# Optimization experiments

Measured on AMD Instinct MI355X. Metric: run time of the kernel, lower is better.

The kernel has to match this reference:

```python
import jax, jax.numpy as jnp
import numpy as np

T, Z, D_DIM = 8, 2048, 1024
N_EXP, P_SLOT, H = 64, 32, 1024
LN_EPS = 1e-5


def setup_inputs() -> dict:
    key = jax.random.key(0)
    k = jax.random.split(key, 5)
    s = 0.02
    return {
        "x": jax.random.normal(k[0], (T, Z, D_DIM), dtype=jnp.float32),
        "phi_w": jax.random.normal(k[1], (N_EXP * P_SLOT, D_DIM), dtype=jnp.float32) * s,
        "phi_b": jax.random.normal(k[2], (N_EXP * P_SLOT,), dtype=jnp.float32) * s,
        "expert_w": jax.random.normal(k[3], (N_EXP, D_DIM, H), dtype=jnp.float32) * s,
        "expert_b": jax.random.normal(k[4], (N_EXP, H), dtype=jnp.float32) * s,
    }


def reference(x, phi_w, phi_b, expert_w, expert_b):
    t, z, d = x.shape
    n = expert_w.shape[0]
    p = phi_w.shape[0] // n
    # routing logits: [t, z, n, p]
    logits = (jnp.einsum('tzd,ed->tze', x, phi_w) + phi_b).reshape(t, z, n, p)
    D = jax.nn.softmax(logits, axis=3)  # dispatch: softmax over slots p
    C = jax.nn.softmax(logits, axis=2)  # combine:  softmax over experts n
    # slot inputs, summed over batch AND tokens (as in the source einsum)
    X_tilde = jnp.einsum('tznp,tzd->npd', D, x)
    X_tilde = jnp.clip(X_tilde, -33000.0, 65000.0)
    # layer norm over last dim, no affine
    mu = jnp.mean(X_tilde, axis=-1, keepdims=True)
    var = jnp.mean(jnp.square(X_tilde - mu), axis=-1, keepdims=True)
    X_tilde = (X_tilde - mu) * jax.lax.rsqrt(var + LN_EPS)
    X_tilde = jnp.tanh(X_tilde)
    # per-expert Linear, batched over experts: [n,p,d] x [n,d,H] -> [n,p,H]
    Y_tilde = jnp.einsum('npd,ndH->npH', X_tilde, expert_w) + expert_b[:, None, :]
    # combine back to tokens: [t,z,H]
    Y = jnp.einsum('tznp,npH->tzH', C, Y_tilde)
    return Y
```

## Files before the change

### kernel.cpp

```cpp
#include <hip/hip_runtime.h>
#include <hip/hip_bf16.h>
#include <math.h>

#define TOKENS   16384
#define DDIM     1024
#define NEXP     64
#define PSLOT    32
#define NSLOTS   2048
#define HDIM     1024
#define LN_EPS   1e-5f
#define KSPLIT   8

typedef __bf16 b16x8 __attribute__((ext_vector_type(8)));
typedef float  f32x4 __attribute__((ext_vector_type(4)));

__device__ __forceinline__ unsigned short f2b(float f) {
    union { float f; unsigned u; } v; v.f = f;
    unsigned r = v.u + 0x7FFF + ((v.u >> 16) & 1);
    return (unsigned short)(r >> 16);
}

__device__ __forceinline__ void load_lds16(const void* g, void* l) {
    __builtin_amdgcn_global_load_lds(
        (const __attribute__((address_space(1))) void*)g,
        (__attribute__((address_space(3))) void*)l, 16, 0, 0);
}

template<bool BIAS>
__global__ __launch_bounds__(512, 2) void gemm_nt_256(
    const unsigned short* __restrict__ A,
    const unsigned short* __restrict__ B,
    const float* __restrict__ bias,
    float* __restrict__ C,
    int M, int N, int K)
{
    __shared__ unsigned short lds[2][2][256 * 64];
    const int tid  = threadIdx.x;
    const int wave = tid >> 6;
    const int lane = tid & 63;
    const int wr = wave >> 2;
    const int wc = wave & 3;
    const int fr = lane & 15;
    const int fs = lane >> 4;
    const int kswz = ((lane & 7) ^ (lane >> 3)) * 8;

    const int gx  = (int)gridDim.x, gy = (int)gridDim.y;
    const int nwg = gx * gy;
    const int wg  = (int)blockIdx.y * gx + (int)blockIdx.x;
    const int swz = (wg & 7) * (nwg >> 3) + (wg >> 3);
    const int m0 = (swz / gx) * 256;
    const int n0 = (swz % gx) * 256;

    const int kc = K / gridDim.z;
    const int kb = blockIdx.z * kc;
    C += (size_t)blockIdx.z * M * N;
    const int NT = kc >> 6;

    f32x4 acc[8][4] = {};
    b16x8 Ag[4][2], Bf[2][2], Bs2[2][2];

#define KOF(T)   (kb + (T) * 64)

#define STAGE_A(BUF, T, R0) { \
    const int k0_ = KOF(T); \
    _Pragma("unroll") for (int hh = 0; hh < 2; ++hh) { \
        const int rp_ = (R0) + hh * 64 + wave * 8 + (lane >> 3); \
        const int L_  = ((rp_ >> 6) & 1) * 128 + ((rp_ >> 7) & 1) * 64 + (rp_ & 63); \
        load_lds16(A + (size_t)(m0 + L_) * K + k0_ + kswz, \
                   &lds[BUF][0][((R0) + hh * 64 + wave * 8) * 64]); } }

#define STAGE_B(BUF, T, R0) { \
    const int k0_ = KOF(T); \
    _Pragma("unroll") for (int hh = 0; hh < 2; ++hh) { \
        const int rp_ = (R0) + hh * 64 + wave * 8 + (lane >> 3); \
        const int L_  = ((rp_ >> 5) & 3) * 64 + ((rp_ >> 7) & 1) * 32 + (rp_ & 31); \
        load_lds16(B + (size_t)(n0 + L_) * K + k0_ + kswz, \
                   &lds[BUF][1][((R0) + hh * 64 + wave * 8) * 64]); } }

#define LDA_G(BUF, IBASE) \
    _Pragma("unroll") for (int ii = 0; ii < 4; ++ii) { \
        const int rp_ = (IBASE) + 64 * wr + ii * 16 + fr; \
        _Pragma("unroll") for (int h = 0; h < 2; ++h) \
            Ag[ii][h] = *(const b16x8*)&lds[BUF][0][rp_ * 64 + (((h * 4 + fs) ^ (rp_ & 7)) * 8)]; }

#define LDB_G(BUF, JBASE, DST) \
    _Pragma("unroll") for (int jj = 0; jj < 2; ++jj) { \
        const int rp_ = (JBASE) + 32 * wc + jj * 16 + fr; \
        _Pragma("unroll") for (int h = 0; h < 2; ++h) \
            DST[jj][h] = *(const b16x8*)&lds[BUF][1][rp_ * 64 + (((h * 4 + fs) ^ (rp_ & 7)) * 8)]; }

#define MFMA_Q(IB, JB, BREG) \
    __builtin_amdgcn_s_setprio(1); \
    _Pragma("unroll") for (int ii = 0; ii < 4; ++ii) \
    _Pragma("unroll") for (int jj = 0; jj < 2; ++jj) \
    _Pragma("unroll") for (int h = 0; h < 2; ++h) \
        acc[(IB) + ii][(JB) + jj] = __builtin_amdgcn_mfma_f32_16x16x32_bf16( \
            Ag[ii][h], BREG[jj][h], acc[(IB) + ii][(JB) + jj], 0, 0, 0); \
    __builtin_amdgcn_s_setprio(0);

#define BAR1  { __builtin_amdgcn_s_barrier(); __builtin_amdgcn_sched_barrier(0); }
#define BAR2  { __builtin_amdgcn_s_barrier(); }
#define VMW6  { asm volatile("s_waitcnt vmcnt(6)" ::: "memory"); \
                __builtin_amdgcn_sched_barrier(0); }
#define VMW0  { asm volatile("s_waitcnt vmcnt(0)" ::: "memory"); \
                __builtin_amdgcn_sched_barrier(0); }

    STAGE_A(0, 0, 0);   STAGE_B(0, 0, 0);   STAGE_B(0, 0, 128);  STAGE_A(0, 0, 128);
    STAGE_A(1, 1, 0);   STAGE_B(1, 1, 0);   STAGE_B(1, 1, 128);
    VMW6; BAR2;

    const int nit = NT >> 1;
    for (int it = 0; it < nit - 1; ++it) {
        const int t1 = 2 * it + 1;
        LDA_G(0, 0); LDB_G(0, 0, Bf);
        STAGE_A(1, t1, 128);
        BAR1; MFMA_Q(0, 0, Bf); BAR2;
        LDB_G(0, 128, Bs2);
        STAGE_A(0, t1 + 1, 0);
        BAR1; MFMA_Q(0, 2, Bs2); BAR2;
        LDA_G(0, 128);
        STAGE_B(0, t1 + 1, 0);
        BAR1; MFMA_Q(4, 2, Bs2); BAR2;
        STAGE_B(0, t1 + 1, 128);
        BAR1; MFMA_Q(4, 0, Bf); VMW6; BAR2;
        LDA_G(1, 0); LDB_G(1, 0, Bf);
        STAGE_A(0, t1 + 1, 128);
        BAR1; MFMA_Q(0, 0, Bf); BAR2;
        LDB_G(1, 128, Bs2);
        STAGE_A(1, t1 + 2, 0);
        BAR1; MFMA_Q(0, 2, Bs2); BAR2;
        LDA_G(1, 128);
        STAGE_B(1, t1 + 2, 0);
        BAR1; MFMA_Q(4, 2, Bs2); BAR2;
        STAGE_B(1, t1 + 2, 128);
        BAR1; MFMA_Q(4, 0, Bf); VMW6; BAR2;
    }

    {
        const int t1 = NT - 1;
        LDA_G(0, 0); LDB_G(0, 0, Bf);
        STAGE_A(1, t1, 128);
        BAR1; MFMA_Q(0, 0, Bf); BAR2;
        LDB_G(0, 128, Bs2);
        BAR1; MFMA_Q(0, 2, Bs2); BAR2;
        LDA_G(0, 128);
        BAR1; MFMA_Q(4, 2, Bs2); BAR2;
        BAR1; MFMA_Q(4, 0, Bf); VMW0; BAR2;
        LDA_G(1, 0); LDB_G(1, 0, Bf);
        BAR1; MFMA_Q(0, 0, Bf); BAR2;
        LDB_G(1, 128, Bs2);
        BAR1; MFMA_Q(0, 2, Bs2); BAR2;
        LDA_G(1, 128);
        BAR1; MFMA_Q(4, 2, Bs2); BAR2;
        BAR1; MFMA_Q(4, 0, Bf); BAR2;
    }

    const int col  = lane & 15;
    const int row4 = (lane >> 4) * 4;
#pragma unroll
    for (int j = 0; j < 4; ++j) {
        const int n = n0 + wc * 64 + j * 16 + col;
        const float bj = BIAS ? bias[n] : 0.f;
#pragma unroll
        for (int i = 0; i < 8; ++i) {
#pragma unroll
            for (int r = 0; r < 4; ++r) {
                const int m = m0 + wr * 128 + i * 16 + row4 + r;
                C[(size_t)m * N + n] = acc[i][j][r] + bj;
            }
        }
    }
#undef KOF
#undef STAGE_A
#undef STAGE_B
#undef LDA_G
#undef LDB_G
#undef MFMA_Q
#undef BAR1
#undef BAR2
#undef VMW6
#undef VMW0
}

__global__ __launch_bounds__(256) void prep_x(
    const float* __restrict__ in, unsigned short* __restrict__ xb,
    unsigned short* __restrict__ xT)
{
    __shared__ unsigned short tile[64][68];
    const int t  = threadIdx.x;
    const int c0 = blockIdx.x * 64;
    const int r0 = blockIdx.y * 64;
    const int tr = t >> 4, tc4 = (t & 15) * 4;
#pragma unroll
    for (int i = 0; i < 4; ++i) {
        const int r = tr + i * 16;
        const float4 v = *(const float4*)&in[(size_t)(r0 + r) * DDIM + c0 + tc4];
        ushort4 o;
        o.x = f2b(v.x); o.y = f2b(v.y); o.z = f2b(v.z); o.w = f2b(v.w);
        *(ushort4*)&xb[(size_t)(r0 + r) * DDIM + c0 + tc4] = o;
        tile[tc4 + 0][r] = o.x; tile[tc4 + 1][r] = o.y;
        tile[tc4 + 2][r] = o.z; tile[tc4 + 3][r] = o.w;
    }
    __syncthreads();
#pragma unroll
    for (int i = 0; i < 4; ++i) {
        const int r = tr + i * 16;
        ushort4 o;
        o.x = tile[r][tc4 + 0]; o.y = tile[r][tc4 + 1];
        o.z = tile[r][tc4 + 2]; o.w = tile[r][tc4 + 3];
        *(ushort4*)&xT[(size_t)(c0 + r) * TOKENS + r0 + tc4] = o;
    }
}

__global__ __launch_bounds__(256) void cast_f32_bf16(
    const float* __restrict__ in, unsigned short* __restrict__ out)
{
    const size_t i = (size_t)(blockIdx.x * 256 + threadIdx.x) * 8;
    const float4 a = *(const float4*)&in[i];
    const float4 b = *(const float4*)&in[i + 4];
    ushort4 o0, o1;
    o0.x = f2b(a.x); o0.y = f2b(a.y); o0.z = f2b(a.z); o0.w = f2b(a.w);
    o1.x = f2b(b.x); o1.y = f2b(b.y); o1.z = f2b(b.z); o1.w = f2b(b.w);
    *(ushort4*)&out[i]     = o0;
    *(ushort4*)&out[i + 4] = o1;
}

__global__ __launch_bounds__(256) void softmax_both(
    const float* __restrict__ logits,
    unsigned short* __restrict__ DbT, unsigned short* __restrict__ Cb)
{
    __shared__ float ls[8][32][33];
    __shared__ float Mv[32][33], Sv[32][33];
    const int tid  = threadIdx.x;
    const int tok0 = blockIdx.x * 32;
    const int tok  = tid & 31;

    {
        const int tk = tid >> 3, pp = (tid & 7) * 4;
#pragma unroll
        for (int q = 0; q < 4; ++q) { Mv[tk][pp + q] = -1e30f; Sv[tk][pp + q] = 0.f; }
    }
    __syncthreads();

    for (int c = 0; c < 8; ++c) {
#pragma unroll
        for (int i = 0; i < 8; ++i) {
            const int flat = i * 256 + tid;
            const int row  = flat >> 6;
            const int c4   = (flat & 63) * 4;
            const float4 v = *(const float4*)&logits[(size_t)(tok0 + row) * NSLOTS + c * 256 + c4];
            float* b = &ls[c4 >> 5][row][c4 & 31];
            b[0] = v.x; b[1] = v.y; b[2] = v.z; b[3] = v.w;
        }
        __syncthreads();

        {
            const int nl = tid >> 5;
            const float* r = ls[nl][tok];
            float m = r[0];
#pragma unroll
            for (int p = 1; p < PSLOT; ++p) m = fmaxf(m, r[p]);
            float s = 0.f;
#pragma unroll
            for (int p = 0; p < PSLOT; ++p) s += __expf(r[p] - m);
            const float inv = 1.f / s;
            unsigned short* o = &DbT[(size_t)(c * 256 + nl * 32) * TOKENS + tok0 + tok];
#pragma unroll
            for (int p = 0; p < PSLOT; ++p)
                o[(size_t)p * TOKENS] = f2b(__expf(r[p] - m) * inv);
        }

        {
            const int pg = tid >> 5;
#pragma unroll
            for (int k = 0; k < 4; ++k) {
                const int p = pg * 4 + k;
                float m8 = ls[0][tok][p];
#pragma unroll
                for (int n = 1; n < 8; ++n) m8 = fmaxf(m8, ls[n][tok][p]);
                float s8 = 0.f;
#pragma unroll
                for (int n = 0; n < 8; ++n) s8 += __expf(ls[n][tok][p] - m8);
                const float M = Mv[tok][p], S = Sv[tok][p];
                const float Mn = fmaxf(M, m8);
                Sv[tok][p] = S * __expf(M - Mn) + s8 * __expf(m8 - Mn);
                Mv[tok][p] = Mn;
            }
        }
        __syncthreads();
    }

    {
        const int tk = tid >> 3, pp = (tid & 7) * 4;
#pragma unroll
        for (int q = 0; q < 4; ++q) Sv[tk][pp + q] = 1.f / Sv[tk][pp + q];
    }
    __syncthreads();

    for (int c = 0; c < 8; ++c) {
#pragma unroll
        for (int i = 0; i < 8; ++i) {
            const int flat = i * 256 + tid;
            const int row  = flat >> 6;
            const int c4   = (flat & 63) * 4;
            const int p    = c4 & 31;
            const float4 v = *(const float4*)&logits[(size_t)(tok0 + row) * NSLOTS + c * 256 + c4];
            ushort4 o;
            o.x = f2b(__expf(v.x - Mv[row][p + 0]) * Sv[row][p + 0]);
            o.y = f2b(__expf(v.y - Mv[row][p + 1]) * Sv[row][p + 1]);
            o.z = f2b(__expf(v.z - Mv[row][p + 2]) * Sv[row][p + 2]);
            o.w = f2b(__expf(v.w - Mv[row][p + 3]) * Sv[row][p + 3]);
            *(ushort4*)&Cb[(size_t)(tok0 + row) * NSLOTS + c * 256 + c4] = o;
        }
    }
}

__global__ __launch_bounds__(256) void reduce_ln_tanh(
    const float* __restrict__ parts, float* __restrict__ Xt)
{
    const int tid = threadIdx.x;
    const size_t off = (size_t)blockIdx.x * DDIM + tid * 4;
    __shared__ float red1[4], red2[4];

    float4 v = *(const float4*)&parts[off];
#pragma unroll
    for (int s = 1; s < KSPLIT; ++s) {
        const float4 p = *(const float4*)&parts[(size_t)s * NSLOTS * DDIM + off];
        v.x += p.x; v.y += p.y; v.z += p.z; v.w += p.w;
    }
    v.x = fminf(fmaxf(v.x, -33000.f), 65000.f);
    v.y = fminf(fmaxf(v.y, -33000.f), 65000.f);
    v.z = fminf(fmaxf(v.z, -33000.f), 65000.f);
    v.w = fminf(fmaxf(v.w, -33000.f), 65000.f);

    float s = v.x + v.y + v.z + v.w;
#pragma unroll
    for (int off2 = 32; off2 > 0; off2 >>= 1) s += __shfl_down(s, off2);
    if ((tid & 63) == 0) red1[tid >> 6] = s;
    __syncthreads();
    const float mu = (red1[0] + red1[1] + red1[2] + red1[3]) * (1.f / DDIM);

    const float dx = v.x - mu, dy = v.y - mu, dz = v.z - mu, dw = v.w - mu;
    float q = dx * dx + dy * dy + dz * dz + dw * dw;
#pragma unroll
    for (int off2 = 32; off2 > 0; off2 >>= 1) q += __shfl_down(q, off2);
    if ((tid & 63) == 0) red2[tid >> 6] = q;
    __syncthreads();
    const float var = (red2[0] + red2[1] + red2[2] + red2[3]) * (1.f / DDIM);
    const float sc = rsqrtf(var + LN_EPS);

    float4 o;
    o.x = tanhf(dx * sc); o.y = tanhf(dy * sc);
    o.z = tanhf(dz * sc); o.w = tanhf(dw * sc);
    *(float4*)&Xt[off] = o;
}

__global__ __launch_bounds__(256) void expert_gemm(
    const float* __restrict__ Xt, const float* __restrict__ W,
    const float* __restrict__ bias, unsigned short* __restrict__ YtT)
{
    const int n   = blockIdx.y;
    const int h0  = blockIdx.x * 64;
    const int tid = threadIdx.x;
    __shared__ float As[32][17];
    __shared__ float Bs[16][68];
    __shared__ unsigned short ty[64][36];

    const int r  = tid >> 3;
    const int c8 = (tid & 7) * 8;
    float acc[8];
#pragma unroll
    for (int j = 0; j < 8; ++j) acc[j] = 0.f;

    const float* Wn = W + (size_t)n * DDIM * HDIM;
    for (int k0 = 0; k0 < DDIM; k0 += 16) {
        if (tid < 128) {
            const int row = tid >> 2, c4 = (tid & 3) * 4;
            const float4 v = *(const float4*)&Xt[(size_t)(n * 32 + row) * DDIM + k0 + c4];
            As[row][c4 + 0] = v.x; As[row][c4 + 1] = v.y;
            As[row][c4 + 2] = v.z; As[row][c4 + 3] = v.w;
        }
        {
            const int row = tid >> 4, c4 = (tid & 15) * 4;
            *(float4*)&Bs[row][c4] =
                *(const float4*)&Wn[(size_t)(k0 + row) * HDIM + h0 + c4];
        }
        __syncthreads();
#pragma unroll
        for (int kk = 0; kk < 16; ++kk) {
            const float a = As[r][kk];
            const float4 b0 = *(const float4*)&Bs[kk][c8];
            const float4 b1 = *(const float4*)&Bs[kk][c8 + 4];
            acc[0] = fmaf(a, b0.x, acc[0]); acc[1] = fmaf(a, b0.y, acc[1]);
            acc[2] = fmaf(a, b0.z, acc[2]); acc[3] = fmaf(a, b0.w, acc[3]);
            acc[4] = fmaf(a, b1.x, acc[4]); acc[5] = fmaf(a, b1.y, acc[5]);
            acc[6] = fmaf(a, b1.z, acc[6]); acc[7] = fmaf(a, b1.w, acc[7]);
        }
        __syncthreads();
    }

    const float* bn = bias + (size_t)n * HDIM + h0;
#pragma unroll
    for (int j = 0; j < 8; ++j)
        ty[c8 + j][r] = f2b(acc[j] + bn[c8 + j]);
    __syncthreads();

    const int row = tid >> 2, q = (tid & 3) * 8;
    const ushort4 u0 = *(const ushort4*)&ty[row][q];
    const ushort4 u1 = *(const ushort4*)&ty[row][q + 4];
    unsigned short* dst = &YtT[(size_t)(h0 + row) * NSLOTS + n * 32 + q];
    *(ushort4*)&dst[0] = u0;
    *(ushort4*)&dst[4] = u1;
}

extern "C" void kernel_launch(void* const* d_in, const int* in_sizes, int n_in,
                              void* d_out, int out_size, void* d_ws, size_t ws_size,
                              hipStream_t stream)
{
    const float* x        = (const float*)d_in[0];
    const float* phi_w    = (const float*)d_in[1];
    const float* phi_b    = (const float*)d_in[2];
    const float* expert_w = (const float*)d_in[3];
    const float* expert_b = (const float*)d_in[4];
    float* out = (float*)d_out;

    char* ws = (char*)d_ws;
    const size_t MB = 1u << 20;
    unsigned short* xb     = (unsigned short*)(ws);
    unsigned short* xT     = (unsigned short*)(ws +  32 * MB);
    unsigned short* pwb    = (unsigned short*)(ws +  64 * MB);
    float*          logits = (float*)(ws +  68 * MB);
    unsigned short* DbT    = (unsigned short*)(ws + 196 * MB);
    unsigned short* Cb     = (unsigned short*)(ws + 260 * MB);
    float*          parts  = (float*)(ws + 324 * MB);
    float*          Xt     = (float*)(ws + 388 * MB);
    unsigned short* YtT    = (unsigned short*)(ws + 396 * MB);

    prep_x<<<dim3(DDIM / 64, TOKENS / 64), 256, 0, stream>>>(x, xb, xT);
    cast_f32_bf16<<<NSLOTS * DDIM / (256 * 8), 256, 0, stream>>>(phi_w, pwb);

    gemm_nt_256<true><<<dim3(NSLOTS / 256, TOKENS / 256), 512, 0, stream>>>(
        xb, pwb, phi_b, logits, TOKENS, NSLOTS, DDIM);

    softmax_both<<<TOKENS / 32, 256, 0, stream>>>(logits, DbT, Cb);

    gemm_nt_256<false>
        <<<dim3(DDIM / 256, NSLOTS / 256, KSPLIT), 512, 0, stream>>>(
            DbT, xT, nullptr, parts, NSLOTS, DDIM, TOKENS);

    reduce_ln_tanh<<<NSLOTS, 256, 0, stream>>>(parts, Xt);

    expert_gemm<<<dim3(HDIM / 64, NEXP), 256, 0, stream>>>(
        Xt, expert_w, expert_b, YtT);

    gemm_nt_256<false><<<dim3(HDIM / 256, TOKENS / 256), 512, 0, stream>>>(
        Cb, YtT, nullptr, out, TOKENS, HDIM, NSLOTS);
}
```

Measured before the change: 767.4 us.

## Store routing logits as bf16 and double-buffer expert GEMM with direct LDS loads

The logits GEMM now writes bf16 instead of fp32, and the softmax kernel reads bf16 and widens it. This halves the 128MB logits write and its two reads. Separately, the expert GEMM tile grows to 32x128 with a K-step of 32, and it uses double-buffered global_load_lds staging with explicit vmcnt waits to overlap loads with FMA work. The cost is reduced logit precision before both softmaxes, plus more LDS and register use in the expert kernel.

```diff
diff --git a/kernel.cpp b/kernel.cpp
--- a/kernel.cpp
+++ b/kernel.cpp
@@ -19,6 +19,9 @@
     unsigned r = v.u + 0x7FFF + ((v.u >> 16) & 1);
     return (unsigned short)(r >> 16);
 }
+__device__ __forceinline__ float b2f(unsigned short u) {
+    union { unsigned u; float f; } v; v.u = ((unsigned)u) << 16; return v.f;
+}
 
 __device__ __forceinline__ void load_lds16(const void* g, void* l) {
     __builtin_amdgcn_global_load_lds(
@@ -26,12 +29,12 @@
         (__attribute__((address_space(3))) void*)l, 16, 0, 0);
 }
 
-template<bool BIAS>
+template<bool BIAS, typename OT>
 __global__ __launch_bounds__(512, 2) void gemm_nt_256(
     const unsigned short* __restrict__ A,
     const unsigned short* __restrict__ B,
     const float* __restrict__ bias,
-    float* __restrict__ C,
+    OT* __restrict__ C,
     int M, int N, int K)
 {
     __shared__ unsigned short lds[2][2][256 * 64];
@@ -166,7 +169,9 @@
 #pragma unroll
             for (int r = 0; r < 4; ++r) {
                 const int m = m0 + wr * 128 + i * 16 + row4 + r;
-                C[(size_t)m * N + n] = acc[i][j][r] + bj;
+                const float v = acc[i][j][r] + bj;
+                if constexpr (sizeof(OT) == 2) C[(size_t)m * N + n] = f2b(v);
+                else                            C[(size_t)m * N + n] = v;
             }
         }
     }
@@ -226,7 +231,7 @@
 }
 
 __global__ __launch_bounds__(256) void softmax_both(
-    const float* __restrict__ logits,
+    const unsigned short* __restrict__ logits,
     unsigned short* __restrict__ DbT, unsigned short* __restrict__ Cb)
 {
     __shared__ float ls[8][32][33];
@@ -244,13 +249,16 @@
 
     for (int c = 0; c < 8; ++c) {
 #pragma unroll
-        for (int i = 0; i < 8; ++i) {
+        for (int i = 0; i < 4; ++i) {
             const int flat = i * 256 + tid;
-            const int row  = flat >> 6;
-            const int c4   = (flat & 63) * 4;
-            const float4 v = *(const float4*)&logits[(size_t)(tok0 + row) * NSLOTS + c * 256 + c4];
-            float* b = &ls[c4 >> 5][row][c4 & 31];
-            b[0] = v.x; b[1] = v.y; b[2] = v.z; b[3] = v.w;
+            const int row  = flat >> 5;
+            const int c8   = (flat & 31) * 8;
+            const unsigned short* p = &logits[(size_t)(tok0 + row) * NSLOTS + c * 256 + c8];
+            const ushort4 u0 = *(const ushort4*)&p[0];
+            const ushort4 u1 = *(const ushort4*)&p[4];
+            float* b = &ls[c8 >> 5][row][c8 & 31];
+            b[0] = b2f(u0.x); b[1] = b2f(u0.y); b[2] = b2f(u0.z); b[3] = b2f(u0.w);
+            b[4] = b2f(u1.x); b[5] = b2f(u1.y); b[6] = b2f(u1.z); b[7] = b2f(u1.w);
         }
         __syncthreads();
 
@@ -299,18 +307,26 @@
 
     for (int c = 0; c < 8; ++c) {
 #pragma unroll
-        for (int i = 0; i < 8; ++i) {
+        for (int i = 0; i < 4; ++i) {
             const int flat = i * 256 + tid;
-            const int row  = flat >> 6;
-            const int c4   = (flat & 63) * 4;
-            const int p    = c4 & 31;
-            const float4 v = *(const float4*)&logits[(size_t)(tok0 + row) * NSLOTS + c * 256 + c4];
-            ushort4 o;
-            o.x = f2b(__expf(v.x - Mv[row][p + 0]) * Sv[row][p + 0]);
-            o.y = f2b(__expf(v.y - Mv[row][p + 1]) * Sv[row][p + 1]);
-            o.z = f2b(__expf(v.z - Mv[row][p + 2]) * Sv[row][p + 2]);
-            o.w = f2b(__expf(v.w - Mv[row][p + 3]) * Sv[row][p + 3]);
-            *(ushort4*)&Cb[(size_t)(tok0 + row) * NSLOTS + c * 256 + c4] = o;
+            const int row  = flat >> 5;
+            const int c8   = (flat & 31) * 8;
+            const int p    = c8 & 31;
+            const unsigned short* q = &logits[(size_t)(tok0 + row) * NSLOTS + c * 256 + c8];
+            const ushort4 u0 = *(const ushort4*)&q[0];
+            const ushort4 u1 = *(const ushort4*)&q[4];
+            ushort4 o0, o1;
+            o0.x = f2b(__expf(b2f(u0.x) - Mv[row][p + 0]) * Sv[row][p + 0]);
+            o0.y = f2b(__expf(b2f(u0.y) - Mv[row][p + 1]) * Sv[row][p + 1]);
+            o0.z = f2b(__expf(b2f(u0.z) - Mv[row][p + 2]) * Sv[row][p + 2]);
+            o0.w = f2b(__expf(b2f(u0.w) - Mv[row][p + 3]) * Sv[row][p + 3]);
+            o1.x = f2b(__expf(b2f(u1.x) - Mv[row][p + 4]) * Sv[row][p + 4]);
+            o1.y = f2b(__expf(b2f(u1.y) - Mv[row][p + 5]) * Sv[row][p + 5]);
+            o1.z = f2b(__expf(b2f(u1.z) - Mv[row][p + 6]) * Sv[row][p + 6]);
+            o1.w = f2b(__expf(b2f(u1.w) - Mv[row][p + 7]) * Sv[row][p + 7]);
+            unsigned short* d = &Cb[(size_t)(tok0 + row) * NSLOTS + c * 256 + c8];
+            *(ushort4*)&d[0] = o0;
+            *(ushort4*)&d[4] = o1;
         }
     }
 }
@@ -360,57 +376,75 @@
     const float* __restrict__ bias, unsigned short* __restrict__ YtT)
 {
     const int n   = blockIdx.y;
-    const int h0  = blockIdx.x * 64;
+    const int h0  = blockIdx.x * 128;
     const int tid = threadIdx.x;
-    __shared__ float As[32][17];
-    __shared__ float Bs[16][68];
-    __shared__ unsigned short ty[64][36];
-
-    const int r  = tid >> 3;
-    const int c8 = (tid & 7) * 8;
-    float acc[8];
-#pragma unroll
-    for (int j = 0; j < 8; ++j) acc[j] = 0.f;
+    __shared__ float As[2][32][32];
+    __shared__ float Bs[2][32][128];
+    __shared__ unsigned short ty[128][36];
+
+    const int r  = tid >> 4;
+    const int c8 = (tid & 15) * 8;
+    float acc0[8], acc1[8];
+#pragma unroll
+    for (int j = 0; j < 8; ++j) { acc0[j] = 0.f; acc1[j] = 0.f; }
 
     const float* Wn = W + (size_t)n * DDIM * HDIM;
-    for (int k0 = 0; k0 < DDIM; k0 += 16) {
-        if (tid < 128) {
-            const int row = tid >> 2, c4 = (tid & 3) * 4;
-            const float4 v = *(const float4*)&Xt[(size_t)(n * 32 + row) * DDIM + k0 + c4];
-            As[row][c4 + 0] = v.x; As[row][c4 + 1] = v.y;
-            As[row][c4 + 2] = v.z; As[row][c4 + 3] = v.w;
-        }
-        {
-            const int row = tid >> 4, c4 = (tid & 15) * 4;
-            *(float4*)&Bs[row][c4] =
-                *(const float4*)&Wn[(size_t)(k0 + row) * HDIM + h0 + c4];
-        }
-        __syncthreads();
-#pragma unroll
-        for (int kk = 0; kk < 16; ++kk) {
-            const float a = As[r][kk];
-            const float4 b0 = *(const float4*)&Bs[kk][c8];
-            const float4 b1 = *(const float4*)&Bs[kk][c8 + 4];
-            acc[0] = fmaf(a, b0.x, acc[0]); acc[1] = fmaf(a, b0.y, acc[1]);
-            acc[2] = fmaf(a, b0.z, acc[2]); acc[3] = fmaf(a, b0.w, acc[3]);
-            acc[4] = fmaf(a, b1.x, acc[4]); acc[5] = fmaf(a, b1.y, acc[5]);
-            acc[6] = fmaf(a, b1.z, acc[6]); acc[7] = fmaf(a, b1.w, acc[7]);
-        }
-        __syncthreads();
-    }
+    const float* Xn = Xt + (size_t)n * 32 * DDIM;
+
+#define EG_STAGE(T, BUF) { \
+    const int k0_ = (T) * 32; \
+    _Pragma("unroll") for (int i = 0; i < 4; ++i) { \
+        const int flat = i * 256 + tid; \
+        const int brow = flat >> 5, bch = (flat & 31) * 4; \
+        load_lds16(Wn + (size_t)(k0_ + brow) * HDIM + h0 + bch, \
+                   &Bs[BUF][brow][bch]); } \
+    { const int arow = tid >> 3, ach = (tid & 7) * 4; \
+      load_lds16(Xn + (size_t)arow * DDIM + k0_ + ach, &As[BUF][arow][ach]); } }
+
+    EG_STAGE(0, 0);
+    for (int t = 0; t < 32; ++t) {
+        const int buf = t & 1;
+        if (t < 31) {
+            EG_STAGE(t + 1, (t + 1) & 1);
+            asm volatile("s_waitcnt vmcnt(5)" ::: "memory");
+        } else {
+            asm volatile("s_waitcnt vmcnt(0)" ::: "memory");
+        }
+        __builtin_amdgcn_sched_barrier(0);
+        __builtin_amdgcn_s_barrier();
+#pragma unroll
+        for (int kk = 0; kk < 32; ++kk) {
+            const float a0 = As[buf][r][kk];
+            const float a1 = As[buf][r + 16][kk];
+            const float4 b0 = *(const float4*)&Bs[buf][kk][c8];
+            const float4 b1 = *(const float4*)&Bs[buf][kk][c8 + 4];
+            acc0[0] = fmaf(a0, b0.x, acc0[0]); acc0[1] = fmaf(a0, b0.y, acc0[1]);
+            acc0[2] = fmaf(a0, b0.z, acc0[2]); acc0[3] = fmaf(a0, b0.w, acc0[3]);
+            acc0[4] = fmaf(a0, b1.x, acc0[4]); acc0[5] = fmaf(a0, b1.y, acc0[5]);
+            acc0[6] = fmaf(a0, b1.z, acc0[6]); acc0[7] = fmaf(a0, b1.w, acc0[7]);
+            acc1[0] = fmaf(a1, b0.x, acc1[0]); acc1[1] = fmaf(a1, b0.y, acc1[1]);
+            acc1[2] = fmaf(a1, b0.z, acc1[2]); acc1[3] = fmaf(a1, b0.w, acc1[3]);
+            acc1[4] = fmaf(a1, b1.x, acc1[4]); acc1[5] = fmaf(a1, b1.y, acc1[5]);
+            acc1[6] = fmaf(a1, b1.z, acc1[6]); acc1[7] = fmaf(a1, b1.w, acc1[7]);
+        }
+        __builtin_amdgcn_s_barrier();
+    }
+#undef EG_STAGE
 
     const float* bn = bias + (size_t)n * HDIM + h0;
 #pragma unroll
-    for (int j = 0; j < 8; ++j)
-        ty[c8 + j][r] = f2b(acc[j] + bn[c8 + j]);
-    __syncthreads();
-
-    const int row = tid >> 2, q = (tid & 3) * 8;
-    const ushort4 u0 = *(const ushort4*)&ty[row][q];
-    const ushort4 u1 = *(const ushort4*)&ty[row][q + 4];
+    for (int j = 0; j < 8; ++j) {
+        const float bj = bn[c8 + j];
+        ty[c8 + j][r]      = f2b(acc0[j] + bj);
+        ty[c8 + j][r + 16] = f2b(acc1[j] + bj);
+    }
+    __syncthreads();
+
+    const int row = tid >> 1, q = (tid & 1) * 16;
     unsigned short* dst = &YtT[(size_t)(h0 + row) * NSLOTS + n * 32 + q];
-    *(ushort4*)&dst[0] = u0;
-    *(ushort4*)&dst[4] = u1;
+#pragma unroll
+    for (int u = 0; u < 4; ++u)
+        *(ushort4*)&dst[u * 4] = *(const ushort4*)&ty[row][q + u * 4];
 }
 
 extern "C" void kernel_launch(void* const* d_in, const int* in_sizes, int n_in,
@@ -429,30 +463,32 @@
     unsigned short* xb     = (unsigned short*)(ws);
     unsigned short* xT     = (unsigned short*)(ws +  32 * MB);
     unsigned short* pwb    = (unsigned short*)(ws +  64 * MB);
-    float*          logits = (float*)(ws +  68 * MB);
-    unsigned short* DbT    = (unsigned short*)(ws + 196 * MB);
-    unsigned short* Cb     = (unsigned short*)(ws + 260 * MB);
-    float*          parts  = (float*)(ws + 324 * MB);
-    float*          Xt     = (float*)(ws + 388 * MB);
-    unsigned short* YtT    = (unsigned short*)(ws + 396 * MB);
+    unsigned short* logbf  = (unsigned short*)(ws +  68 * MB);
+    unsigned short* DbT    = (unsigned short*)(ws + 132 * MB);
+    unsigned short* Cb     = (unsigned short*)(ws + 196 * MB);
+    float*          parts  = (float*)(ws + 260 * MB);
+    float*          Xt     = (float*)(ws + 324 * MB);
+    unsigned short* YtT    = (unsigned short*)(ws + 332 * MB);
 
     prep_x<<<dim3(DDIM / 64, TOKENS / 64), 256, 0, stream>>>(x, xb, xT);
     cast_f32_bf16<<<NSLOTS * DDIM / (256 * 8), 256, 0, stream>>>(phi_w, pwb);
 
-    gemm_nt_256<true><<<dim3(NSLOTS / 256, TOKENS / 256), 512, 0, stream>>>(
-        xb, pwb, phi_b, logits, TOKENS, NSLOTS, DDIM);
-
-    softmax_both<<<TOKENS / 32, 256, 0, stream>>>(logits, DbT, Cb);
-
-    gemm_nt_256<false>
+    gemm_nt_256<true, unsigned short>
+        <<<dim3(NSLOTS / 256, TOKENS / 256), 512, 0, stream>>>(
+            xb, pwb, phi_b, logbf, TOKENS, NSLOTS, DDIM);
+
+    softmax_both<<<TOKENS / 32, 256, 0, stream>>>(logbf, DbT, Cb);
+
+    gemm_nt_256<false, float>
         <<<dim3(DDIM / 256, NSLOTS / 256, KSPLIT), 512, 0, stream>>>(
             DbT, xT, nullptr, parts, NSLOTS, DDIM, TOKENS);
 
     reduce_ln_tanh<<<NSLOTS, 256, 0, stream>>>(parts, Xt);
 
-    expert_gemm<<<dim3(HDIM / 64, NEXP), 256, 0, stream>>>(
+    expert_gemm<<<dim3(HDIM / 128, NEXP), 256, 0, stream>>>(
         Xt, expert_w, expert_b, YtT);
 
-    gemm_nt_256<false><<<dim3(HDIM / 256, TOKENS / 256), 512, 0, stream>>>(
-        Cb, YtT, nullptr, out, TOKENS, HDIM, NSLOTS);
-}
+    gemm_nt_256<false, float>
+        <<<dim3(HDIM / 256, TOKENS / 256), 512, 0, stream>>>(
+            Cb, YtT, nullptr, out, TOKENS, HDIM, NSLOTS);
+}
```

New measurement: 733.7 us. 4.4% less time.
